# Optimization experiments

Hardware: AMD Instinct MI355X
Metric: run time of the kernel (lower is better)

The kernel has to match this reference:

```python
import jax, jax.numpy as jnp
import numpy as np

B, S, K, D = 2, 2048, 8, 1024
P, KP, DFF = 32, 4, 4096


def setup_inputs() -> dict:
    key = jax.random.key(0)
    ks = jax.random.split(key, 17)
    s = 0.02
    return {
        "x": jax.random.normal(ks[0], (B, S, D), jnp.float32),
        "router_out": jax.random.normal(ks[1], (B, S, D), jnp.float32),
        "topk_neuron_idx": jax.random.randint(ks[2], (B, S, K), 0, 512, jnp.int32),
        "topk_neuron_weights": jax.random.uniform(ks[3], (B, S, K), jnp.float32),
        "selected_neurons": jax.random.normal(ks[4], (B, S, K, D), jnp.float32),
        "context": jax.random.normal(ks[5], (B, S, D), jnp.float32),
        "Wq": jax.random.normal(ks[6], (D, D), jnp.float32) * s,
        "bq": jnp.zeros((D,), jnp.float32),
        "Wk": jax.random.normal(ks[7], (D, D), jnp.float32) * s,
        "bk": jnp.zeros((D,), jnp.float32),
        "Wv": jax.random.normal(ks[8], (D, D), jnp.float32) * s,
        "bv": jnp.zeros((D,), jnp.float32),
        "pattern_queries": jax.random.normal(ks[9], (P, D), jnp.float32) * s,
        "Wup": jax.random.normal(ks[10], (DFF, D), jnp.float32) * s,
        "bup": jnp.zeros((DFF,), jnp.float32),
        "Wdown": jax.random.normal(ks[11], (D, DFF), jnp.float32) * s,
        "bdown": jnp.zeros((D,), jnp.float32),
    }


def reference(x, router_out, topk_neuron_idx, topk_neuron_weights,
              selected_neurons, context, Wq, bq, Wk, bk, Wv, bv,
              pattern_queries, Wup, bup, Wdown, bdown):
    scale = 1.0 / jnp.sqrt(jnp.float32(D))
    # K-wide neuron self-attention (per token), torch Linear: y = x @ W.T + b
    q = jnp.einsum('bskd,ed->bske', selected_neurons, Wq) + bq
    kk = jnp.einsum('bskd,ed->bske', selected_neurons, Wk) + bk
    v = jnp.einsum('bskd,ed->bske', selected_neurons, Wv) + bv
    attn = jax.nn.softmax(jnp.einsum('bsqd,bskd->bsqk', q, kk) * scale, axis=-1)
    interacted = jnp.einsum('bsqk,bskd->bsqd', attn, v)  # [B,S,K,D]
    # pattern similarity: [B,S,P,K]
    nps = jnp.einsum('pd,bskd->bspk', pattern_queries, interacted) * scale
    neuron_based = (nps * topk_neuron_weights[:, :, None, :]).sum(-1)  # [B,S,P]
    context_based = jnp.einsum('bsd,pd->bsp', context, pattern_queries)
    pattern_scores = 0.5 * neuron_based + 0.5 * context_based
    topk_scores, topk_idx = jax.lax.top_k(pattern_scores, KP)  # [B,S,KP]
    topk_w = jax.nn.softmax(topk_scores, axis=-1)
    sel_attn = jnp.take_along_axis(nps, topk_idx[..., None], axis=2)  # [B,S,KP,K]
    final_attn = (topk_w[..., None] * jax.nn.softmax(sel_attn, axis=-1)).sum(2)  # [B,S,K]
    aggregated = jnp.einsum('bsk,bskd->bsd', final_attn, interacted)
    combined = x + aggregated
    h = jax.nn.gelu(combined @ Wup.T + bup, approximate=False)
    return h @ Wdown.T + bdown
```

## Files before the change

kernel.cpp:

```cpp
#include <hip/hip_runtime.h>
#include <math.h>

typedef unsigned short ushort_t;
typedef __attribute__((ext_vector_type(8))) short short8;
typedef __attribute__((ext_vector_type(4))) float floatx4;

static __device__ __forceinline__ float bf2f(ushort_t h){
  return __uint_as_float(((unsigned int)h) << 16);
}
static __device__ __forceinline__ ushort_t f2bf(float f){
  unsigned int u = __float_as_uint(f);
  unsigned int r = u + 0x7FFFu + ((u >> 16) & 1u);
  return (ushort_t)(r >> 16);
}
static __device__ __forceinline__ void unpack8(uint4 u, float* f){
  f[0] = __uint_as_float(u.x << 16); f[1] = __uint_as_float(u.x & 0xffff0000u);
  f[2] = __uint_as_float(u.y << 16); f[3] = __uint_as_float(u.y & 0xffff0000u);
  f[4] = __uint_as_float(u.z << 16); f[5] = __uint_as_float(u.z & 0xffff0000u);
  f[6] = __uint_as_float(u.w << 16); f[7] = __uint_as_float(u.w & 0xffff0000u);
}
static __device__ __forceinline__ uint4 pack8(const float* f){
  uint4 u;
  u.x = (unsigned)f2bf(f[0]) | ((unsigned)f2bf(f[1]) << 16);
  u.y = (unsigned)f2bf(f[2]) | ((unsigned)f2bf(f[3]) << 16);
  u.z = (unsigned)f2bf(f[4]) | ((unsigned)f2bf(f[5]) << 16);
  u.w = (unsigned)f2bf(f[6]) | ((unsigned)f2bf(f[7]) << 16);
  return u;
}

static __device__ __forceinline__ void gload16(const void* g, void* l){
  __builtin_amdgcn_global_load_lds((const __attribute__((address_space(1))) void*)g,
                                   (__attribute__((address_space(3))) void*)l, 16, 0, 0);
}

__global__ __launch_bounds__(256) void k_cvt_multi(
    const float* __restrict__ s0, ushort_t* __restrict__ d0, int e0,
    const float* __restrict__ s1, ushort_t* __restrict__ d1, int e1,
    const float* __restrict__ s2, ushort_t* __restrict__ d2, int e2,
    const float* __restrict__ s3, ushort_t* __restrict__ d3, int e3,
    const float* __restrict__ s4, ushort_t* __restrict__ d4, int e4,
    const float* __restrict__ s5, ushort_t* __restrict__ d5, int e5){
  int i = blockIdx.x * 256 + threadIdx.x;
  const float* s; ushort_t* d; int b;
  if      (i < e0){ s = s0; d = d0; b = 0;  }
  else if (i < e1){ s = s1; d = d1; b = e0; }
  else if (i < e2){ s = s2; d = d2; b = e1; }
  else if (i < e3){ s = s3; d = d3; b = e2; }
  else if (i < e4){ s = s4; d = d4; b = e3; }
  else if (i < e5){ s = s5; d = d5; b = e4; }
  else return;
  int j = i - b;
  float4 v = ((const float4*)s)[j];
  unsigned long long p = (unsigned long long)f2bf(v.x)
                       | ((unsigned long long)f2bf(v.y) << 16)
                       | ((unsigned long long)f2bf(v.z) << 32)
                       | ((unsigned long long)f2bf(v.w) << 48);
  ((unsigned long long*)d)[j] = p;
}

__global__ __launch_bounds__(256) void k_transpose3(const float* __restrict__ s0, ushort_t* __restrict__ d0,
                                                    const float* __restrict__ s1, ushort_t* __restrict__ d1,
                                                    const float* __restrict__ s2, ushort_t* __restrict__ d2){
  __shared__ float tile[32][33];
  const float* in; ushort_t* out;
  if      (blockIdx.z == 0){ in = s0; out = d0; }
  else if (blockIdx.z == 1){ in = s1; out = d1; }
  else                     { in = s2; out = d2; }
  int bx = blockIdx.x * 32, by = blockIdx.y * 32;
  int tx = threadIdx.x & 31, ty = threadIdx.x >> 5;
  for (int i = 0; i < 32; i += 8)
    tile[ty + i][tx] = in[(size_t)(by + ty + i) * 1024 + bx + tx];
  __syncthreads();
  for (int i = 0; i < 32; i += 8)
    out[(size_t)(bx + ty + i) * 1024 + by + tx] = f2bf(tile[tx][ty + i]);
}

__global__ __launch_bounds__(256) void k_wvec2(const float* __restrict__ bq,
                                               const ushort_t* __restrict__ WKT,
                                               float* __restrict__ wv){
  int d = (blockIdx.x << 2) + (threadIdx.x >> 6);
  int l = threadIdx.x & 63;
  const uint4* row = (const uint4*)(WKT + (size_t)d * 1024 + (l << 4));
  const float4* b4 = (const float4*)(bq + (l << 4));
  float w[16], bb[16];
  unpack8(row[0], w); unpack8(row[1], w + 8);
#pragma unroll
  for (int i = 0; i < 4; i++){
    float4 v = b4[i];
    bb[i*4] = v.x; bb[i*4+1] = v.y; bb[i*4+2] = v.z; bb[i*4+3] = v.w;
  }
  float a = 0.f;
#pragma unroll
  for (int i = 0; i < 16; i++) a += w[i] * bb[i];
#pragma unroll
  for (int s = 1; s < 64; s <<= 1) a += __shfl_xor(a, s);
  if (l == 0) wv[d] = a;
}

__global__ __launch_bounds__(256) void k_pb2(const float* __restrict__ pat,
                                             const float* __restrict__ bv,
                                             float* __restrict__ pb){
  int p = (blockIdx.x << 2) + (threadIdx.x >> 6);
  int l = threadIdx.x & 63;
  const float4* pr = (const float4*)(pat + p * 1024) + l;
  const float4* b4 = (const float4*)bv + l;
  float a = 0.f;
#pragma unroll
  for (int i = 0; i < 4; i++){
    float4 x = pr[i * 64], y = b4[i * 64];
    a += x.x * y.x + x.y * y.y + x.z * y.z + x.w * y.w;
  }
#pragma unroll
  for (int s = 1; s < 64; s <<= 1) a += __shfl_xor(a, s);
  if (l == 0) pb[p] = a;
}

__global__ __launch_bounds__(256) void k_pv2(const ushort_t* __restrict__ WVT,
                                             const ushort_t* __restrict__ PATB,
                                             ushort_t* __restrict__ PVB){
  int d = (blockIdx.x << 2) + (threadIdx.x >> 6);
  int l = threadIdx.x & 63;
  const uint4* wr = (const uint4*)(WVT + (size_t)d * 1024 + (l << 4));
  float w[16];
  unpack8(wr[0], w); unpack8(wr[1], w + 8);
  for (int p = 0; p < 32; p++){
    const uint4* pr = (const uint4*)(PATB + p * 1024 + (l << 4));
    float pw[16];
    unpack8(pr[0], pw); unpack8(pr[1], pw + 8);
    float a = 0.f;
#pragma unroll
    for (int i = 0; i < 16; i++) a += w[i] * pw[i];
#pragma unroll
    for (int s = 1; s < 64; s <<= 1) a += __shfl_xor(a, s);
    if (l == 0) PVB[p * 1024 + d] = f2bf(a);
  }
}

template<int MODE, int GN>
__global__ __launch_bounds__(256) void k_gemm_bt(const ushort_t* __restrict__ A,
                                                 const ushort_t* __restrict__ B,
                                                 void* __restrict__ C,
                                                 const float* __restrict__ bias,
                                                 const float* __restrict__ Xadd,
                                                 int M, int N, int K){
  (void)M;
  __shared__ ushort_t As[128 * 32];
  __shared__ ushort_t Bs[128 * 32];
  const int tid = threadIdx.x;
  const int w = tid >> 6, l = tid & 63;
  const int id = blockIdx.x;
  const int xcd = id & 7;
  const int t2 = id >> 3;
  const int nt = t2 % GN;
  const int mt = ((t2 / GN) << 3) + xcd;
  const int m0 = mt << 7, n0 = nt << 7;
  const int wm = (w >> 1) << 6, wn = (w & 1) << 6;
  const int rA = (w << 4) + (l >> 2);
  const int cA = (l & 3) << 3;
  const int fr = l & 15, fq = l >> 4;

  floatx4 acc[4][4];
#pragma unroll
  for (int i = 0; i < 4; i++)
#pragma unroll
    for (int j = 0; j < 4; j++) acc[i][j] = (floatx4)0.0f;

  const ushort_t* Ab = A + (size_t)(m0 + rA) * K + cA;
  const ushort_t* Bb = B + (size_t)(n0 + rA) * K + cA;
  const size_t row64 = (size_t)64 * K;
  ushort_t* Asw = As + (w << 9);
  ushort_t* Bsw = Bs + (w << 9);

  for (int k0 = 0; k0 < K; k0 += 32){
    __syncthreads();
    gload16(Ab + k0, Asw);
    gload16(Ab + row64 + k0, Asw + 2048);
    gload16(Bb + k0, Bsw);
    gload16(Bb + row64 + k0, Bsw + 2048);
    __syncthreads();
    short8 af[4], bg[4];
#pragma unroll
    for (int i = 0; i < 4; i++){
      af[i] = *(const short8*)(As + ((wm + (i << 4) + fr) << 5) + (fq << 3));
      bg[i] = *(const short8*)(Bs + ((wn + (i << 4) + fr) << 5) + (fq << 3));
    }
#pragma unroll
    for (int i = 0; i < 4; i++)
#pragma unroll
      for (int j = 0; j < 4; j++)
        acc[i][j] = __builtin_amdgcn_mfma_f32_16x16x32_bf16(af[i], bg[j], acc[i][j], 0, 0, 0);
  }

#pragma unroll
  for (int i = 0; i < 4; i++){
    int row = m0 + wm + (i << 4) + (fq << 2);
#pragma unroll
    for (int j = 0; j < 4; j++){
      int col = n0 + wn + (j << 4) + fr;
      float b = (MODE >= 1) ? bias[col] : 0.0f;
#pragma unroll
      for (int r = 0; r < 4; r++){
        float v = acc[i][j][r] + b;
        size_t idx = (size_t)(row + r) * N + col;
        if (MODE == 2) v += Xadd[idx];
        if (MODE == 3) v = 0.5f * v * (1.0f + erff(v * 0.70710678118654752f));
        if (MODE == 4) ((float*)C)[idx] = v;
        else           ((ushort_t*)C)[idx] = f2bf(v);
      }
    }
  }
}

template<bool ADDB>
__global__ __launch_bounds__(256) void k_gemm_n32(const ushort_t* __restrict__ A,
                                                  const ushort_t* __restrict__ B,
                                                  float* __restrict__ C,
                                                  const float* __restrict__ bvec,
                                                  int M, int K){
  (void)M;
  __shared__ ushort_t As[128 * 32];
  __shared__ ushort_t Bs[32 * 32];
  const int tid = threadIdx.x;
  const int w = tid >> 6, l = tid & 63;
  const int m0 = blockIdx.x << 7;
  const int rA = (w << 4) + (l >> 2);
  const int cA = (l & 3) << 3;
  const int fr = l & 15, fq = l >> 4;

  floatx4 acc[2][2];
#pragma unroll
  for (int i = 0; i < 2; i++)
#pragma unroll
    for (int j = 0; j < 2; j++) acc[i][j] = (floatx4)0.0f;

  const ushort_t* Ab = A + (size_t)(m0 + rA) * K + cA;
  const ushort_t* Bb = B + (size_t)rA * K + cA;
  const size_t row64 = (size_t)64 * K;

  for (int k0 = 0; k0 < K; k0 += 32){
    __syncthreads();
    gload16(Ab + k0, As + (w << 9));
    gload16(Ab + row64 + k0, As + 2048 + (w << 9));
    if (w < 2) gload16(Bb + k0, Bs + (w << 9));
    __syncthreads();
    short8 af[2], bg[2];
#pragma unroll
    for (int i = 0; i < 2; i++)
      af[i] = *(const short8*)(As + (((w << 5) + (i << 4) + fr) << 5) + (fq << 3));
#pragma unroll
    for (int j = 0; j < 2; j++)
      bg[j] = *(const short8*)(Bs + (((j << 4) + fr) << 5) + (fq << 3));
#pragma unroll
    for (int i = 0; i < 2; i++)
#pragma unroll
      for (int j = 0; j < 2; j++)
        acc[i][j] = __builtin_amdgcn_mfma_f32_16x16x32_bf16(af[i], bg[j], acc[i][j], 0, 0, 0);
  }

#pragma unroll
  for (int i = 0; i < 2; i++){
    int row = m0 + (w << 5) + (i << 4) + (fq << 2);
#pragma unroll
    for (int j = 0; j < 2; j++){
      int col = (j << 4) + fr;
      float b = ADDB ? bvec[col] : 0.0f;
#pragma unroll
      for (int r = 0; r < 4; r++)
        C[(size_t)(row + r) * 32 + col] = acc[i][j][r] + b;
    }
  }
}

__global__ __launch_bounds__(256) void k_attn(const ushort_t* __restrict__ T,
                                              const ushort_t* __restrict__ SNB,
                                              const float* __restrict__ NPRE,
                                              const float* __restrict__ CB,
                                              const float* __restrict__ TW,
                                              ushort_t* __restrict__ GSN){
  __shared__ float logit_s[4 * 256];
  __shared__ float attn_s[8 * 64];
  __shared__ float npr_s[8 * 256];
  __shared__ float nps_s[8 * 256];
  __shared__ float sc_s[8 * 32];
  __shared__ float tw_s[8 * 8];
  __shared__ int   sel_s[8 * 4];
  __shared__ float tkw_s[8 * 4], rmax_s[8 * 4], rsum_s[8 * 4], fa_s[8 * 8], g_s[8 * 8];

  const int t = threadIdx.x;
  const int w = t >> 6, l = t & 63;
  const int tok0 = blockIdx.x << 3;
  const int pair = (blockIdx.x << 2) + w;

  {
    const size_t rbase = (size_t)pair * 16 + (l & 15);
    const int ko = (l >> 4) << 3;
    const ushort_t* Ap = T   + rbase * 1024 + ko;
    const ushort_t* Bp = SNB + rbase * 1024 + ko;
    floatx4 acc = (floatx4)0.0f;
#pragma unroll 4
    for (int k0 = 0; k0 < 1024; k0 += 32){
      short8 a = *(const short8*)(Ap + k0);
      short8 b = *(const short8*)(Bp + k0);
      acc = __builtin_amdgcn_mfma_f32_16x16x32_bf16(a, b, acc, 0, 0, 0);
    }
    const int col = l & 15, r0 = (l >> 4) << 2;
#pragma unroll
    for (int r = 0; r < 4; r++)
      logit_s[(w << 8) + (r0 + r) * 16 + col] = acc[r] * 0.03125f;
  }
  {
#pragma unroll
    for (int i = 0; i < 8; i++)
      npr_s[(i << 8) + t] = NPRE[((size_t)tok0 << 8) + (i << 8) + t];
    if (t < 64) tw_s[t] = TW[(tok0 << 3) + t];
  }
  __syncthreads();

  const int loc = t >> 5, q = t & 31;
  if (q < 8){
    const float* lrow = logit_s + ((loc >> 1) << 8) + (loc & 1) * 136 + q * 16;
    float a[8]; float m = -1e30f;
#pragma unroll
    for (int j = 0; j < 8; j++){ a[j] = lrow[j]; m = fmaxf(m, a[j]); }
    float s = 0.f;
#pragma unroll
    for (int j = 0; j < 8; j++){ a[j] = expf(a[j] - m); s += a[j]; }
    float inv = 1.f / s;
#pragma unroll
    for (int j = 0; j < 8; j++) attn_s[(loc << 6) + q * 8 + j] = a[j] * inv;
  }
  __syncthreads();

  {
    const int qq = q & 7, p0 = (q >> 3) << 3;
    float a[8];
#pragma unroll
    for (int k = 0; k < 8; k++) a[k] = attn_s[(loc << 6) + qq * 8 + k];
    const float* np = npr_s + (loc << 8);
    float* npsr = nps_s + (loc << 8);
    for (int p = p0; p < p0 + 8; p++){
      float acc = 0.f;
#pragma unroll
      for (int k = 0; k < 8; k++) acc += a[k] * np[k * 32 + p];
      npsr[p * 8 + qq] = acc * 0.03125f;
    }
  }
  __syncthreads();

  {
    const float* npsr = nps_s + (loc << 8);
    float nb = 0.f;
#pragma unroll
    for (int qq = 0; qq < 8; qq++) nb += npsr[q * 8 + qq] * tw_s[(loc << 3) + qq];
    sc_s[(loc << 5) + q] = 0.5f * nb + 0.5f * CB[((size_t)(tok0 + loc) << 5) + q];
  }
  __syncthreads();

  if (q == 0){
    const float* sc = sc_s + (loc << 5);
    unsigned used = 0; float vals[4]; int idx[4];
    for (int kp = 0; kp < 4; kp++){
      float best = -1e30f; int bi = 0;
      for (int p = 0; p < 32; p++)
        if (!((used >> p) & 1u) && sc[p] > best){ best = sc[p]; bi = p; }
      used |= 1u << bi; vals[kp] = best; idx[kp] = bi;
    }
    float mm = vals[0], ss = 0.f, e[4];
    for (int kp = 0; kp < 4; kp++){ e[kp] = expf(vals[kp] - mm); ss += e[kp]; }
    for (int kp = 0; kp < 4; kp++){ tkw_s[(loc << 2) + kp] = e[kp] / ss; sel_s[(loc << 2) + kp] = idx[kp]; }
  }
  __syncthreads();

  if (q < 4){
    const float* npsr = nps_s + (loc << 8);
    int p = sel_s[(loc << 2) + q];
    float mm = -1e30f;
    for (int j = 0; j < 8; j++) mm = fmaxf(mm, npsr[p * 8 + j]);
    float ss = 0.f;
    for (int j = 0; j < 8; j++) ss += expf(npsr[p * 8 + j] - mm);
    rmax_s[(loc << 2) + q] = mm; rsum_s[(loc << 2) + q] = ss;
  }
  __syncthreads();

  if (q < 8){
    const float* npsr = nps_s + (loc << 8);
    float f = 0.f;
    for (int kp = 0; kp < 4; kp++){
      int p = sel_s[(loc << 2) + kp];
      f += tkw_s[(loc << 2) + kp] * expf(npsr[p * 8 + q] - rmax_s[(loc << 2) + kp]) / rsum_s[(loc << 2) + kp];
    }
    fa_s[(loc << 3) + q] = f;
  }
  __syncthreads();

  if (q < 8){
    float g = 0.f;
    for (int qq = 0; qq < 8; qq++) g += fa_s[(loc << 3) + qq] * attn_s[(loc << 6) + qq * 8 + q];
    g_s[(loc << 3) + q] = g;
  }
  __syncthreads();

  for (int tl = 0; tl < 2; tl++){
    const int tkl = (w << 1) + tl;
    const size_t tok = (size_t)tok0 + tkl;
    float o[16];
#pragma unroll
    for (int i = 0; i < 16; i++) o[i] = 0.f;
#pragma unroll
    for (int k = 0; k < 8; k++){
      float gk = g_s[(tkl << 3) + k];
      const uint4* src = (const uint4*)(SNB + ((tok << 3) + k) * 1024 + (l << 4));
      float f0[8], f1[8];
      unpack8(src[0], f0);
      unpack8(src[1], f1);
#pragma unroll
      for (int i = 0; i < 8; i++){ o[i] += gk * f0[i]; o[8 + i] += gk * f1[i]; }
    }
    uint4* dst = (uint4*)(GSN + tok * 1024 + (l << 4));
    dst[0] = pack8(o);
    dst[1] = pack8(o + 8);
  }
}

extern "C" void kernel_launch(void* const* d_in, const int* in_sizes, int n_in,
                              void* d_out, int out_size, void* d_ws, size_t ws_size,
                              hipStream_t stream){
  (void)in_sizes; (void)n_in; (void)out_size; (void)ws_size;
  const float* x   = (const float*)d_in[0];
  const float* tw  = (const float*)d_in[3];
  const float* SN  = (const float*)d_in[4];
  const float* ctx = (const float*)d_in[5];
  const float* Wq  = (const float*)d_in[6];
  const float* bq  = (const float*)d_in[7];
  const float* Wk  = (const float*)d_in[8];
  const float* Wv  = (const float*)d_in[10];
  const float* bv  = (const float*)d_in[11];
  const float* pat = (const float*)d_in[12];
  const float* Wup = (const float*)d_in[13];
  const float* bup = (const float*)d_in[14];
  const float* Wdn = (const float*)d_in[15];
  const float* bdn = (const float*)d_in[16];
  float* out = (float*)d_out;

  char* ws = (char*)d_ws;
  size_t off = 0;
  auto alloc = [&](size_t bytes) -> char* {
    char* p = ws + off;
    off = (off + bytes + 255) & ~(size_t)255;
    return p;
  };
  ushort_t* SNB  = (ushort_t*)alloc(67108864);
  ushort_t* TB   = (ushort_t*)alloc(67108864);
  float*    NPRE = (float*)alloc(4194304);
  float*    CBb  = (float*)alloc(524288);
  ushort_t* GSN  = (ushort_t*)alloc(8388608);
  ushort_t* CTXB = (ushort_t*)alloc(8388608);
  ushort_t* PATB = (ushort_t*)alloc(65536);
  ushort_t* WVB  = (ushort_t*)alloc(2097152);
  ushort_t* WUPB = (ushort_t*)alloc(8388608);
  ushort_t* WDNB = (ushort_t*)alloc(8388608);
  ushort_t* ATB  = (ushort_t*)alloc(2097152);
  ushort_t* WKTB = (ushort_t*)alloc(2097152);
  ushort_t* WQTB = (ushort_t*)alloc(2097152);
  ushort_t* WVTB = (ushort_t*)alloc(2097152);
  ushort_t* PVB  = (ushort_t*)alloc(65536);
  float*    WVEC = (float*)alloc(4096);
  float*    PBv  = (float*)alloc(128);
  ushort_t* H    = SNB;
  ushort_t* CMB  = TB;

  const int e0 = 8388608, e1 = e0 + 1048576, e2 = e1 + 8192,
            e3 = e2 + 262144, e4 = e3 + 1048576, e5 = e4 + 1048576;
  k_cvt_multi<<<(e5 + 255) / 256, 256, 0, stream>>>(
      SN, SNB, e0, ctx, CTXB, e1, pat, PATB, e2,
      Wv, WVB, e3, Wup, WUPB, e4, Wdn, WDNB, e5);
  k_transpose3<<<dim3(32, 32, 3), 256, 0, stream>>>(Wq, WQTB, Wk, WKTB, Wv, WVTB);
  k_wvec2<<<256, 256, 0, stream>>>(bq, WKTB, WVEC);
  k_pb2<<<8, 256, 0, stream>>>(pat, bv, PBv);
  k_pv2<<<256, 256, 0, stream>>>(WVTB, PATB, PVB);

  k_gemm_bt<0, 8><<<64, 256, 0, stream>>>(WKTB, WQTB, ATB, nullptr, nullptr, 1024, 1024, 1024);
  k_gemm_bt<1, 8><<<2048, 256, 0, stream>>>(SNB, ATB, TB, WVEC, nullptr, 32768, 1024, 1024);
  k_gemm_n32<true><<<256, 256, 0, stream>>>(SNB, PVB, NPRE, PBv, 32768, 1024);
  k_gemm_n32<false><<<32, 256, 0, stream>>>(CTXB, PATB, CBb, nullptr, 4096, 1024);
  k_attn<<<512, 256, 0, stream>>>(TB, SNB, NPRE, CBb, tw, GSN);
  k_gemm_bt<2, 8><<<256, 256, 0, stream>>>(GSN, WVB, CMB, bv, x, 4096, 1024, 1024);
  k_gemm_bt<3, 32><<<1024, 256, 0, stream>>>(CMB, WUPB, H, bup, nullptr, 4096, 4096, 1024);
  k_gemm_bt<4, 8><<<256, 256, 0, stream>>>(H, WDNB, out, bdn, nullptr, 4096, 1024, 4096);
}
```

Measured before the change: 675.2 us.

## Fuse pattern projection into attention kernel, merge prep kernels, add 64-row GEMM tiles

Removes the separate N=32 GEMM over all 32768 neuron rows that produced NPRE. The pattern-value projection is now computed inside the attention kernel via extra MFMAs that reuse the already-loaded SNB fragments, and the pb bias is added there. This avoids a full re-read of SNB and the NPRE write/read round trip, but adds MFMA work and register pressure inside k_attn. It also merges three small prep kernels into one launch and uses 64-row GEMM tiles for the N=1024 GEMMs to double block count and improve occupancy.

```diff
diff --git a/kernel.cpp b/kernel.cpp
--- a/kernel.cpp
+++ b/kernel.cpp
@@ -5,9 +5,6 @@
 typedef __attribute__((ext_vector_type(8))) short short8;
 typedef __attribute__((ext_vector_type(4))) float floatx4;
 
-static __device__ __forceinline__ float bf2f(ushort_t h){
-  return __uint_as_float(((unsigned int)h) << 16);
-}
 static __device__ __forceinline__ ushort_t f2bf(float f){
   unsigned int u = __float_as_uint(f);
   unsigned int r = u + 0x7FFFu + ((u >> 16) & 1u);
@@ -75,64 +72,63 @@
     out[(size_t)(bx + ty + i) * 1024 + by + tx] = f2bf(tile[tx][ty + i]);
 }
 
-__global__ __launch_bounds__(256) void k_wvec2(const float* __restrict__ bq,
-                                               const ushort_t* __restrict__ WKT,
-                                               float* __restrict__ wv){
-  int d = (blockIdx.x << 2) + (threadIdx.x >> 6);
-  int l = threadIdx.x & 63;
-  const uint4* row = (const uint4*)(WKT + (size_t)d * 1024 + (l << 4));
-  const float4* b4 = (const float4*)(bq + (l << 4));
-  float w[16], bb[16];
-  unpack8(row[0], w); unpack8(row[1], w + 8);
-#pragma unroll
-  for (int i = 0; i < 4; i++){
-    float4 v = b4[i];
-    bb[i*4] = v.x; bb[i*4+1] = v.y; bb[i*4+2] = v.z; bb[i*4+3] = v.w;
-  }
-  float a = 0.f;
-#pragma unroll
-  for (int i = 0; i < 16; i++) a += w[i] * bb[i];
-#pragma unroll
-  for (int s = 1; s < 64; s <<= 1) a += __shfl_xor(a, s);
-  if (l == 0) wv[d] = a;
-}
-
-__global__ __launch_bounds__(256) void k_pb2(const float* __restrict__ pat,
-                                             const float* __restrict__ bv,
-                                             float* __restrict__ pb){
-  int p = (blockIdx.x << 2) + (threadIdx.x >> 6);
-  int l = threadIdx.x & 63;
-  const float4* pr = (const float4*)(pat + p * 1024) + l;
-  const float4* b4 = (const float4*)bv + l;
-  float a = 0.f;
-#pragma unroll
-  for (int i = 0; i < 4; i++){
-    float4 x = pr[i * 64], y = b4[i * 64];
-    a += x.x * y.x + x.y * y.y + x.z * y.z + x.w * y.w;
-  }
-#pragma unroll
-  for (int s = 1; s < 64; s <<= 1) a += __shfl_xor(a, s);
-  if (l == 0) pb[p] = a;
-}
-
-__global__ __launch_bounds__(256) void k_pv2(const ushort_t* __restrict__ WVT,
-                                             const ushort_t* __restrict__ PATB,
-                                             ushort_t* __restrict__ PVB){
-  int d = (blockIdx.x << 2) + (threadIdx.x >> 6);
-  int l = threadIdx.x & 63;
-  const uint4* wr = (const uint4*)(WVT + (size_t)d * 1024 + (l << 4));
-  float w[16];
-  unpack8(wr[0], w); unpack8(wr[1], w + 8);
-  for (int p = 0; p < 32; p++){
-    const uint4* pr = (const uint4*)(PATB + p * 1024 + (l << 4));
-    float pw[16];
-    unpack8(pr[0], pw); unpack8(pr[1], pw + 8);
+__global__ __launch_bounds__(256) void k_prep(const float* __restrict__ bq,
+                                              const ushort_t* __restrict__ WKT,
+                                              float* __restrict__ wv,
+                                              const float* __restrict__ pat,
+                                              const float* __restrict__ bv,
+                                              float* __restrict__ pb,
+                                              const ushort_t* __restrict__ WVT,
+                                              const ushort_t* __restrict__ PATB,
+                                              ushort_t* __restrict__ PVB){
+  const int bid = blockIdx.x;
+  const int l = threadIdx.x & 63;
+  if (bid < 256){
+    int d = (bid << 2) + (threadIdx.x >> 6);
+    const uint4* row = (const uint4*)(WKT + (size_t)d * 1024 + (l << 4));
+    const float4* b4 = (const float4*)(bq + (l << 4));
+    float w[16], bb[16];
+    unpack8(row[0], w); unpack8(row[1], w + 8);
+#pragma unroll
+    for (int i = 0; i < 4; i++){
+      float4 v = b4[i];
+      bb[i*4] = v.x; bb[i*4+1] = v.y; bb[i*4+2] = v.z; bb[i*4+3] = v.w;
+    }
     float a = 0.f;
 #pragma unroll
-    for (int i = 0; i < 16; i++) a += w[i] * pw[i];
+    for (int i = 0; i < 16; i++) a += w[i] * bb[i];
 #pragma unroll
     for (int s = 1; s < 64; s <<= 1) a += __shfl_xor(a, s);
-    if (l == 0) PVB[p * 1024 + d] = f2bf(a);
+    if (l == 0) wv[d] = a;
+  } else if (bid < 264){
+    int p = ((bid - 256) << 2) + (threadIdx.x >> 6);
+    const float4* pr = (const float4*)(pat + p * 1024) + l;
+    const float4* b4 = (const float4*)bv + l;
+    float a = 0.f;
+#pragma unroll
+    for (int i = 0; i < 4; i++){
+      float4 x = pr[i * 64], y = b4[i * 64];
+      a += x.x * y.x + x.y * y.y + x.z * y.z + x.w * y.w;
+    }
+#pragma unroll
+    for (int s = 1; s < 64; s <<= 1) a += __shfl_xor(a, s);
+    if (l == 0) pb[p] = a;
+  } else {
+    int d = ((bid - 264) << 2) + (threadIdx.x >> 6);
+    const uint4* wr = (const uint4*)(WVT + (size_t)d * 1024 + (l << 4));
+    float w[16];
+    unpack8(wr[0], w); unpack8(wr[1], w + 8);
+    for (int p = 0; p < 32; p++){
+      const uint4* pr = (const uint4*)(PATB + p * 1024 + (l << 4));
+      float pw[16];
+      unpack8(pr[0], pw); unpack8(pr[1], pw + 8);
+      float a = 0.f;
+#pragma unroll
+      for (int i = 0; i < 16; i++) a += w[i] * pw[i];
+#pragma unroll
+      for (int s = 1; s < 64; s <<= 1) a += __shfl_xor(a, s);
+      if (l == 0) PVB[p * 1024 + d] = f2bf(a);
+    }
   }
 }
 
@@ -142,8 +138,7 @@
                                                  void* __restrict__ C,
                                                  const float* __restrict__ bias,
                                                  const float* __restrict__ Xadd,
-                                                 int M, int N, int K){
-  (void)M;
+                                                 int N, int K){
   __shared__ ushort_t As[128 * 32];
   __shared__ ushort_t Bs[128 * 32];
   const int tid = threadIdx.x;
@@ -211,13 +206,82 @@
   }
 }
 
-template<bool ADDB>
+template<int MODE, int GN>
+__global__ __launch_bounds__(256) void k_gemm_bt64(const ushort_t* __restrict__ A,
+                                                   const ushort_t* __restrict__ B,
+                                                   void* __restrict__ C,
+                                                   const float* __restrict__ bias,
+                                                   const float* __restrict__ Xadd,
+                                                   int N, int K){
+  __shared__ ushort_t As[64 * 32];
+  __shared__ ushort_t Bs[128 * 32];
+  const int tid = threadIdx.x;
+  const int w = tid >> 6, l = tid & 63;
+  const int id = blockIdx.x;
+  const int xcd = id & 7;
+  const int t2 = id >> 3;
+  const int nt = t2 % GN;
+  const int mt = ((t2 / GN) << 3) + xcd;
+  const int m0 = mt << 6, n0 = nt << 7;
+  const int wm = (w >> 1) << 5, wn = (w & 1) << 6;
+  const int rA = (w << 4) + (l >> 2);
+  const int cA = (l & 3) << 3;
+  const int fr = l & 15, fq = l >> 4;
+
+  floatx4 acc[2][4];
+#pragma unroll
+  for (int i = 0; i < 2; i++)
+#pragma unroll
+    for (int j = 0; j < 4; j++) acc[i][j] = (floatx4)0.0f;
+
+  const ushort_t* Ab = A + (size_t)(m0 + rA) * K + cA;
+  const ushort_t* Bb = B + (size_t)(n0 + rA) * K + cA;
+  const size_t row64 = (size_t)64 * K;
+
+  for (int k0 = 0; k0 < K; k0 += 32){
+    __syncthreads();
+    gload16(Ab + k0, As + (w << 9));
+    gload16(Bb + k0, Bs + (w << 9));
+    gload16(Bb + row64 + k0, Bs + 2048 + (w << 9));
+    __syncthreads();
+    short8 af[2], bg[4];
+#pragma unroll
+    for (int i = 0; i < 2; i++)
+      af[i] = *(const short8*)(As + ((wm + (i << 4) + fr) << 5) + (fq << 3));
+#pragma unroll
+    for (int j = 0; j < 4; j++)
+      bg[j] = *(const short8*)(Bs + ((wn + (j << 4) + fr) << 5) + (fq << 3));
+#pragma unroll
+    for (int i = 0; i < 2; i++)
+#pragma unroll
+      for (int j = 0; j < 4; j++)
+        acc[i][j] = __builtin_amdgcn_mfma_f32_16x16x32_bf16(af[i], bg[j], acc[i][j], 0, 0, 0);
+  }
+
+#pragma unroll
+  for (int i = 0; i < 2; i++){
+    int row = m0 + wm + (i << 4) + (fq << 2);
+#pragma unroll
+    for (int j = 0; j < 4; j++){
+      int col = n0 + wn + (j << 4) + fr;
+      float b = (MODE >= 1) ? bias[col] : 0.0f;
+#pragma unroll
+      for (int r = 0; r < 4; r++){
+        float v = acc[i][j][r] + b;
+        size_t idx = (size_t)(row + r) * N + col;
+        if (MODE == 2) v += Xadd[idx];
+        if (MODE == 3) v = 0.5f * v * (1.0f + erff(v * 0.70710678118654752f));
+        if (MODE == 4) ((float*)C)[idx] = v;
+        else           ((ushort_t*)C)[idx] = f2bf(v);
+      }
+    }
+  }
+}
+
 __global__ __launch_bounds__(256) void k_gemm_n32(const ushort_t* __restrict__ A,
                                                   const ushort_t* __restrict__ B,
                                                   float* __restrict__ C,
-                                                  const float* __restrict__ bvec,
-                                                  int M, int K){
-  (void)M;
+                                                  int K){
   __shared__ ushort_t As[128 * 32];
   __shared__ ushort_t Bs[32 * 32];
   const int tid = threadIdx.x;
@@ -263,17 +327,17 @@
 #pragma unroll
     for (int j = 0; j < 2; j++){
       int col = (j << 4) + fr;
-      float b = ADDB ? bvec[col] : 0.0f;
 #pragma unroll
       for (int r = 0; r < 4; r++)
-        C[(size_t)(row + r) * 32 + col] = acc[i][j][r] + b;
+        C[(size_t)(row + r) * 32 + col] = acc[i][j][r];
     }
   }
 }
 
 __global__ __launch_bounds__(256) void k_attn(const ushort_t* __restrict__ T,
                                               const ushort_t* __restrict__ SNB,
-                                              const float* __restrict__ NPRE,
+                                              const ushort_t* __restrict__ PVB,
+                                              const float* __restrict__ PBv,
                                               const float* __restrict__ CB,
                                               const float* __restrict__ TW,
                                               ushort_t* __restrict__ GSN){
@@ -283,6 +347,7 @@
   __shared__ float nps_s[8 * 256];
   __shared__ float sc_s[8 * 32];
   __shared__ float tw_s[8 * 8];
+  __shared__ float pb_s[32];
   __shared__ int   sel_s[8 * 4];
   __shared__ float tkw_s[8 * 4], rmax_s[8 * 4], rsum_s[8 * 4], fa_s[8 * 8], g_s[8 * 8];
 
@@ -296,24 +361,29 @@
     const int ko = (l >> 4) << 3;
     const ushort_t* Ap = T   + rbase * 1024 + ko;
     const ushort_t* Bp = SNB + rbase * 1024 + ko;
-    floatx4 acc = (floatx4)0.0f;
+    const ushort_t* P0 = PVB + (size_t)(l & 15) * 1024 + ko;
+    const ushort_t* P1 = P0 + 16 * 1024;
+    floatx4 aL = (floatx4)0.0f, aP0 = (floatx4)0.0f, aP1 = (floatx4)0.0f;
 #pragma unroll 4
     for (int k0 = 0; k0 < 1024; k0 += 32){
-      short8 a = *(const short8*)(Ap + k0);
       short8 b = *(const short8*)(Bp + k0);
-      acc = __builtin_amdgcn_mfma_f32_16x16x32_bf16(a, b, acc, 0, 0, 0);
+      aL  = __builtin_amdgcn_mfma_f32_16x16x32_bf16(*(const short8*)(Ap + k0), b, aL, 0, 0, 0);
+      aP0 = __builtin_amdgcn_mfma_f32_16x16x32_bf16(*(const short8*)(P0 + k0), b, aP0, 0, 0, 0);
+      aP1 = __builtin_amdgcn_mfma_f32_16x16x32_bf16(*(const short8*)(P1 + k0), b, aP1, 0, 0, 0);
     }
     const int col = l & 15, r0 = (l >> 4) << 2;
 #pragma unroll
     for (int r = 0; r < 4; r++)
-      logit_s[(w << 8) + (r0 + r) * 16 + col] = acc[r] * 0.03125f;
-  }
-  {
-#pragma unroll
-    for (int i = 0; i < 8; i++)
-      npr_s[(i << 8) + t] = NPRE[((size_t)tok0 << 8) + (i << 8) + t];
-    if (t < 64) tw_s[t] = TW[(tok0 << 3) + t];
-  }
+      logit_s[(w << 8) + (r0 + r) * 16 + col] = aL[r] * 0.03125f;
+    const int tokloc = (w << 1) + (col >> 3), kk = col & 7;
+#pragma unroll
+    for (int r = 0; r < 4; r++){
+      npr_s[(tokloc << 8) + kk * 32 + (r0 + r)]      = aP0[r];
+      npr_s[(tokloc << 8) + kk * 32 + (r0 + r) + 16] = aP1[r];
+    }
+  }
+  if (t < 64) tw_s[t] = TW[(tok0 << 3) + t];
+  if (t < 32) pb_s[t] = PBv[t];
   __syncthreads();
 
   const int loc = t >> 5, q = t & 31;
@@ -339,7 +409,7 @@
     const float* np = npr_s + (loc << 8);
     float* npsr = nps_s + (loc << 8);
     for (int p = p0; p < p0 + 8; p++){
-      float acc = 0.f;
+      float acc = pb_s[p];
 #pragma unroll
       for (int k = 0; k < 8; k++) acc += a[k] * np[k * 32 + p];
       npsr[p * 8 + qq] = acc * 0.03125f;
@@ -451,7 +521,6 @@
   };
   ushort_t* SNB  = (ushort_t*)alloc(67108864);
   ushort_t* TB   = (ushort_t*)alloc(67108864);
-  float*    NPRE = (float*)alloc(4194304);
   float*    CBb  = (float*)alloc(524288);
   ushort_t* GSN  = (ushort_t*)alloc(8388608);
   ushort_t* CTXB = (ushort_t*)alloc(8388608);
@@ -475,16 +544,13 @@
       SN, SNB, e0, ctx, CTXB, e1, pat, PATB, e2,
       Wv, WVB, e3, Wup, WUPB, e4, Wdn, WDNB, e5);
   k_transpose3<<<dim3(32, 32, 3), 256, 0, stream>>>(Wq, WQTB, Wk, WKTB, Wv, WVTB);
-  k_wvec2<<<256, 256, 0, stream>>>(bq, WKTB, WVEC);
-  k_pb2<<<8, 256, 0, stream>>>(pat, bv, PBv);
-  k_pv2<<<256, 256, 0, stream>>>(WVTB, PATB, PVB);
-
-  k_gemm_bt<0, 8><<<64, 256, 0, stream>>>(WKTB, WQTB, ATB, nullptr, nullptr, 1024, 1024, 1024);
-  k_gemm_bt<1, 8><<<2048, 256, 0, stream>>>(SNB, ATB, TB, WVEC, nullptr, 32768, 1024, 1024);
-  k_gemm_n32<true><<<256, 256, 0, stream>>>(SNB, PVB, NPRE, PBv, 32768, 1024);
-  k_gemm_n32<false><<<32, 256, 0, stream>>>(CTXB, PATB, CBb, nullptr, 4096, 1024);
-  k_attn<<<512, 256, 0, stream>>>(TB, SNB, NPRE, CBb, tw, GSN);
-  k_gemm_bt<2, 8><<<256, 256, 0, stream>>>(GSN, WVB, CMB, bv, x, 4096, 1024, 1024);
-  k_gemm_bt<3, 32><<<1024, 256, 0, stream>>>(CMB, WUPB, H, bup, nullptr, 4096, 4096, 1024);
-  k_gemm_bt<4, 8><<<256, 256, 0, stream>>>(H, WDNB, out, bdn, nullptr, 4096, 1024, 4096);
-}
+  k_prep<<<520, 256, 0, stream>>>(bq, WKTB, WVEC, pat, bv, PBv, WVTB, PATB, PVB);
+
+  k_gemm_bt64<0, 8><<<128, 256, 0, stream>>>(WKTB, WQTB, ATB, nullptr, nullptr, 1024, 1024);
+  k_gemm_bt<1, 8><<<2048, 256, 0, stream>>>(SNB, ATB, TB, WVEC, nullptr, 1024, 1024);
+  k_gemm_n32<<<32, 256, 0, stream>>>(CTXB, PATB, CBb, 1024);
+  k_attn<<<512, 256, 0, stream>>>(TB, SNB, PVB, PBv, CBb, tw, GSN);
+  k_gemm_bt64<2, 8><<<512, 256, 0, stream>>>(GSN, WVB, CMB, bv, x, 1024, 1024);
+  k_gemm_bt<3, 32><<<1024, 256, 0, stream>>>(CMB, WUPB, H, bup, nullptr, 4096, 1024);
+  k_gemm_bt64<4, 8><<<512, 256, 0, stream>>>(H, WDNB, out, bdn, nullptr, 1024, 4096);
+}
```

Result: faster. 630.5 us (-6.6%).
